# Kernel optimization log

Hardware: AMD Instinct MI355X
Metric: run time of the kernel (lower is better)

## Reference

```python
import jax, jax.numpy as jnp
import numpy as np

NUM_NODES = 100000
NUM_EDGES = 3200000
NHEADS = 8


def setup_inputs() -> dict:
    key = jax.random.key(0)
    k1, k2 = jax.random.split(key)
    edge_scores = jax.random.normal(k1, (NUM_EDGES, NHEADS, 1), dtype=jnp.float32)
    dst = jax.random.randint(k2, (NUM_EDGES,), 0, NUM_NODES, dtype=jnp.int32)
    gain = jnp.ones((NHEADS, 1), dtype=jnp.float32)
    bias = jnp.zeros((NHEADS, 1), dtype=jnp.float32)
    return {"edge_scores": edge_scores, "gain": gain, "bias": bias,
            "dst": dst, "num_nodes": NUM_NODES}


def reference(edge_scores, gain, bias, dst, num_nodes):
    # Per-destination-node mean/std normalization of incoming-edge scores
    # (EdgeNorm), then per-head gain/bias.
    # edge_scores: (E, H, 1); dst: (E,) int; gain/bias: (H, 1)
    ones = jnp.ones_like(edge_scores)
    counts = jax.ops.segment_sum(ones, dst, num_segments=num_nodes)        # (N,H,1)
    sums = jax.ops.segment_sum(edge_scores, dst, num_segments=num_nodes)   # (N,H,1)
    means = sums / jnp.maximum(counts, 1.0)
    residual = edge_scores - means[dst]                                    # (E,H,1)
    var_sum = jax.ops.segment_sum(residual * residual, dst, num_segments=num_nodes)
    stdev = jnp.sqrt(var_sum / counts)  # NaN only at zero-degree nodes (never gathered)
    inv_stdev = 1.0 / jnp.maximum(stdev, 1e-5)                             # (N,H,1)
    normalized = residual * inv_stdev[dst]                                 # (E,H,1)
    return gain * normalized + bias
```

## Files before the change

kernel.cpp:

```cpp
#include <hip/hip_runtime.h>


#define NHEADS  8
#define KSHIFT  9
#define KNODES  512
#define NNODES  100000
#define NB      196
#define CBLK    2048
#define CHMAX   1600
#define PARTS   8
#define SLMAX   2560
#define ACCW    17

__global__ __launch_bounds__(256)
void count_kernel(const int* __restrict__ dst, unsigned* __restrict__ counts,
                  int p0, int p1, int chunk) {
    __shared__ unsigned hist[NB];
    for (int i = threadIdx.x; i < NB; i += 256) hist[i] = 0u;
    __syncthreads();
    const int blk = blockIdx.x;
    const int s0 = p0 + blk * chunk;
    const int s1 = min(s0 + chunk, p1);
    for (int i = s0 + (int)threadIdx.x * 4; i < s1; i += 256 * 4) {
        if (i + 4 <= s1) {
            int4 d = *reinterpret_cast<const int4*>(dst + i);
            atomicAdd(&hist[(unsigned)d.x >> KSHIFT], 1u);
            atomicAdd(&hist[(unsigned)d.y >> KSHIFT], 1u);
            atomicAdd(&hist[(unsigned)d.z >> KSHIFT], 1u);
            atomicAdd(&hist[(unsigned)d.w >> KSHIFT], 1u);
        } else {
            for (int j = i; j < s1; ++j)
                atomicAdd(&hist[(unsigned)dst[j] >> KSHIFT], 1u);
        }
    }
    __syncthreads();
    for (int b = threadIdx.x; b < NB; b += 256)
        counts[(size_t)b * CBLK + blk] = hist[b];
}

__global__ __launch_bounds__(256)
void scan_kernel(unsigned* __restrict__ counts, unsigned* __restrict__ totals) {
    __shared__ unsigned sc[256];
    const int b = blockIdx.x;
    const size_t base = (size_t)b * CBLK + (size_t)threadIdx.x * 8;
    uint4 v0 = *reinterpret_cast<uint4*>(counts + base);
    uint4 v1 = *reinterpret_cast<uint4*>(counts + base + 4);
    unsigned s = v0.x + v0.y + v0.z + v0.w + v1.x + v1.y + v1.z + v1.w;
    sc[threadIdx.x] = s;
    __syncthreads();
    for (int off = 1; off < 256; off <<= 1) {
        unsigned t = (threadIdx.x >= (unsigned)off) ? sc[threadIdx.x - off] : 0u;
        __syncthreads();
        sc[threadIdx.x] += t;
        __syncthreads();
    }
    unsigned e = sc[threadIdx.x] - s;
    uint4 o0, o1;
    o0.x = e;            o0.y = o0.x + v0.x;
    o0.z = o0.y + v0.y;  o0.w = o0.z + v0.z;
    o1.x = o0.w + v0.w;  o1.y = o1.x + v1.x;
    o1.z = o1.y + v1.y;  o1.w = o1.z + v1.z;
    *reinterpret_cast<uint4*>(counts + base) = o0;
    *reinterpret_cast<uint4*>(counts + base + 4) = o1;
    if (threadIdx.x == 255) totals[b] = sc[255];
}

__global__ __launch_bounds__(256)
void base_kernel(const unsigned* __restrict__ totals, unsigned* __restrict__ base) {
    __shared__ unsigned sc[256];
    unsigned v = (threadIdx.x < NB) ? totals[threadIdx.x] : 0u;
    sc[threadIdx.x] = v;
    __syncthreads();
    for (int off = 1; off < 256; off <<= 1) {
        unsigned t = (threadIdx.x >= (unsigned)off) ? sc[threadIdx.x - off] : 0u;
        __syncthreads();
        sc[threadIdx.x] += t;
        __syncthreads();
    }
    if (threadIdx.x < NB) base[threadIdx.x] = sc[threadIdx.x] - v;
}

__global__ __launch_bounds__(256)
void scatter_kernel(const int* __restrict__ dst,
                    const unsigned* __restrict__ counts,
                    const unsigned* __restrict__ base,
                    const float* __restrict__ scores,
                    float* __restrict__ payload,
                    unsigned short* __restrict__ nidx,
                    int p0, int p1, int chunk, unsigned capE) {
    __shared__ unsigned hist[256];
    __shared__ unsigned pfx[NB];
    __shared__ unsigned lofs[NB];
    __shared__ unsigned gbase[NB];
    __shared__ unsigned ord[CHMAX];
    const int blk = blockIdx.x;
    const int s0 = p0 + blk * chunk;
    const int s1 = min(s0 + chunk, p1);
    const int n  = s1 - s0;

    hist[threadIdx.x] = 0u;
    __syncthreads();
    for (int i = s0 + (int)threadIdx.x * 4; i < s1; i += 256 * 4) {
        if (i + 4 <= s1) {
            int4 d = *reinterpret_cast<const int4*>(dst + i);
            atomicAdd(&hist[(unsigned)d.x >> KSHIFT], 1u);
            atomicAdd(&hist[(unsigned)d.y >> KSHIFT], 1u);
            atomicAdd(&hist[(unsigned)d.z >> KSHIFT], 1u);
            atomicAdd(&hist[(unsigned)d.w >> KSHIFT], 1u);
        } else {
            for (int j = i; j < s1; ++j)
                atomicAdd(&hist[(unsigned)dst[j] >> KSHIFT], 1u);
        }
    }
    __syncthreads();
    unsigned myc = hist[threadIdx.x];
    for (int off = 1; off < 256; off <<= 1) {
        unsigned t = (threadIdx.x >= (unsigned)off) ? hist[threadIdx.x - off] : 0u;
        __syncthreads();
        hist[threadIdx.x] += t;
        __syncthreads();
    }
    unsigned excl = hist[threadIdx.x] - myc;
    if (threadIdx.x < NB) {
        pfx[threadIdx.x]  = excl;
        lofs[threadIdx.x] = excl;
        gbase[threadIdx.x] =
            base[threadIdx.x] + counts[(size_t)threadIdx.x * CBLK + blk];
    }
    __syncthreads();
    for (int i = s0 + (int)threadIdx.x; i < s1; i += 256) {
        int d = dst[i];
        unsigned b = (unsigned)d >> KSHIFT;
        unsigned pos = atomicAdd(&lofs[b], 1u);
        if (pos < (unsigned)CHMAX)
            ord[pos] = (unsigned)(i - s0) |
                       ((unsigned)(d & (KNODES - 1)) << 12) | (b << 21);
    }
    __syncthreads();
    for (int p = (int)threadIdx.x; p < n; p += 256) {
        unsigned r = ord[p];
        int el       = (int)(r & 0xFFFu);
        unsigned nib = (r >> 12) & 0x1FFu;
        unsigned b   = r >> 21;
        unsigned gi  = gbase[b] + (unsigned)p - pfx[b];
        if (gi >= capE) continue;
        const float4* ps = reinterpret_cast<const float4*>(
            scores + (size_t)(s0 + el) * NHEADS);
        float4 x0 = ps[0], x1 = ps[1];
        float4* pd = reinterpret_cast<float4*>(payload + (size_t)gi * NHEADS);
        pd[0] = x0;
        pd[1] = x1;
        nidx[gi] = (unsigned short)nib;
    }
}

__global__ __launch_bounds__(512)
void stats_kernel(const float* __restrict__ payload,
                  const unsigned short* __restrict__ nidx,
                  const unsigned* __restrict__ totals,
                  const unsigned* __restrict__ baseb,
                  float* __restrict__ nodeacc) {
    __shared__ unsigned hist[KNODES];
    __shared__ unsigned seg[KNODES + 1];
    __shared__ unsigned cur[KNODES];
    __shared__ unsigned sc[512];
    __shared__ unsigned short sidx[SLMAX];

    const int part  = blockIdx.x;
    const int b     = blockIdx.y;
    const int total = (int)totals[b];
    const int rs    = (int)baseb[b];
    const int sliceLen = (total + PARTS - 1) / PARTS;
    const int l0 = min(total, part * sliceLen);
    const int l1 = min(total, l0 + sliceLen);
    const int n  = l1 - l0;
    if (n <= 0) return;
    const int gs0 = rs + l0;

    const int tid = (int)threadIdx.x;
    if (tid < KNODES) hist[tid] = 0u;
    __syncthreads();
    for (int i = tid; i < n; i += 512) {
        if (i >= SLMAX) break;
        unsigned k = (unsigned)nidx[gs0 + i] & (KNODES - 1);
        atomicAdd(&hist[k], 1u);
    }
    __syncthreads();
    unsigned v = hist[tid];
    sc[tid] = v;
    __syncthreads();
    for (int off = 1; off < 512; off <<= 1) {
        unsigned t = (tid >= off) ? sc[tid - off] : 0u;
        __syncthreads();
        sc[tid] += t;
        __syncthreads();
    }
    unsigned excl = sc[tid] - v;
    seg[tid] = excl;
    cur[tid] = excl;
    if (tid == 511) seg[KNODES] = sc[511];
    __syncthreads();
    for (int i = tid; i < n; i += 512) {
        if (i >= SLMAX) break;
        unsigned k = (unsigned)nidx[gs0 + i] & (KNODES - 1);
        unsigned pos = atomicAdd(&cur[k], 1u);
        if (pos < (unsigned)SLMAX) sidx[pos] = (unsigned short)i;
    }
    __syncthreads();

    const int wv   = tid >> 6;
    const int lane = tid & 63;
    const int grp  = lane >> 3;
    const int h    = lane & 7;
    for (int k = wv; k < KNODES; k += 8) {
        int ss = (int)seg[k];
        int ee = (int)seg[k + 1];
        int cc = ee - ss;
        if (cc <= 0) continue;
        float sv = 0.f, sw = 0.f;
        for (int j = grp; j < cc; j += 8) {
            int li = (int)sidx[ss + j];
            float x = payload[(size_t)(gs0 + li) * NHEADS + h];
            sv += x;
            sw = fmaf(x, x, sw);
        }
        sv += __shfl_xor(sv, 8);  sw += __shfl_xor(sw, 8);
        sv += __shfl_xor(sv, 16); sw += __shfl_xor(sw, 16);
        sv += __shfl_xor(sv, 32); sw += __shfl_xor(sw, 32);
        int gnode = b * KNODES + k;
        if (lane < ACCW && gnode < NNODES) {
            float val = (lane < 8) ? sv : ((lane < 16) ? sw : (float)cc);
            atomicAdd(&nodeacc[(size_t)gnode * ACCW + lane], val);
        }
    }
}

__global__ __launch_bounds__(256)
void coeff_kernel(const float* __restrict__ nodeacc,
                  const float* __restrict__ gain,
                  const float* __restrict__ bias,
                  float* __restrict__ AB, int total) {
    int i = blockIdx.x * 256 + threadIdx.x;
    if (i >= total) return;
    int node = i >> 3, h = i & 7;
    const float* acc = nodeacc + (size_t)node * ACCW;
    float s = acc[h];
    float q = acc[8 + h];
    float c = acc[16];
    float cm   = fmaxf(c, 1.0f);
    float mean = s / cm;
    float var  = fmaxf(q - s * mean, 0.0f);
    float inv  = 1.0f / fmaxf(sqrtf(var / cm), 1e-5f);
    float a = gain[h] * inv;
    AB[(size_t)node * 16 + h]     = a;
    AB[(size_t)node * 16 + 8 + h] = fmaf(-a, mean, bias[h]);
}

__global__ __launch_bounds__(256)
void edge_out_kernel(const float* __restrict__ scores,
                     const int* __restrict__ dst,
                     const float* __restrict__ AB,
                     float* __restrict__ out,
                     int num_edges) {
    int e = blockIdx.x * 256 + threadIdx.x;
    if (e >= num_edges) return;
    int d = dst[e];
    const float4* px  = reinterpret_cast<const float4*>(scores + (size_t)e * NHEADS);
    const float4* pab = reinterpret_cast<const float4*>(AB + (size_t)d * 16);
    float4 x0 = px[0], x1 = px[1];
    float4 a0 = pab[0], a1 = pab[1];
    float4 b0 = pab[2], b1 = pab[3];
    float4 o0, o1;
    o0.x = fmaf(a0.x, x0.x, b0.x);
    o0.y = fmaf(a0.y, x0.y, b0.y);
    o0.z = fmaf(a0.z, x0.z, b0.z);
    o0.w = fmaf(a0.w, x0.w, b0.w);
    o1.x = fmaf(a1.x, x1.x, b1.x);
    o1.y = fmaf(a1.y, x1.y, b1.y);
    o1.z = fmaf(a1.z, x1.z, b1.z);
    o1.w = fmaf(a1.w, x1.w, b1.w);
    float4* po = reinterpret_cast<float4*>(out + (size_t)e * NHEADS);
    po[0] = o0;
    po[1] = o1;
}

__global__ void edge_stats_fallback(const float* __restrict__ scores,
                                    const int* __restrict__ dst,
                                    float* __restrict__ sums,
                                    float* __restrict__ sumsq,
                                    int* __restrict__ counts,
                                    int num_edges) {
    int e = blockIdx.x * blockDim.x + threadIdx.x;
    if (e >= num_edges) return;
    int d = dst[e];
    const float4* p = reinterpret_cast<const float4*>(scores + (size_t)e * NHEADS);
    float4 x0 = p[0], x1 = p[1];
    float* s = sums  + (size_t)d * NHEADS;
    float* q = sumsq + (size_t)d * NHEADS;
    atomicAdd(s + 0, x0.x); atomicAdd(s + 1, x0.y);
    atomicAdd(s + 2, x0.z); atomicAdd(s + 3, x0.w);
    atomicAdd(s + 4, x1.x); atomicAdd(s + 5, x1.y);
    atomicAdd(s + 6, x1.z); atomicAdd(s + 7, x1.w);
    atomicAdd(q + 0, x0.x * x0.x); atomicAdd(q + 1, x0.y * x0.y);
    atomicAdd(q + 2, x0.z * x0.z); atomicAdd(q + 3, x0.w * x0.w);
    atomicAdd(q + 4, x1.x * x1.x); atomicAdd(q + 5, x1.y * x1.y);
    atomicAdd(q + 6, x1.z * x1.z); atomicAdd(q + 7, x1.w * x1.w);
    atomicAdd(counts + d, 1);
}

__global__ void coeff_fallback(const float* __restrict__ sums,
                               const float* __restrict__ sumsq,
                               const int* __restrict__ counts,
                               const float* __restrict__ gain,
                               const float* __restrict__ bias,
                               float* __restrict__ AB, int total) {
    int i = blockIdx.x * blockDim.x + threadIdx.x;
    if (i >= total) return;
    int h = i & (NHEADS - 1);
    int node = i >> 3;
    float cm = fmaxf((float)counts[node], 1.0f);
    float s = sums[i];
    float mean = s / cm;
    float var_sum = fmaxf(sumsq[i] - s * mean, 0.0f);
    float inv = 1.0f / fmaxf(sqrtf(var_sum / cm), 1e-5f);
    float a = gain[h] * inv;
    AB[(size_t)node * 16 + h]     = a;
    AB[(size_t)node * 16 + 8 + h] = fmaf(-a, mean, bias[h]);
}

extern "C" void kernel_launch(void* const* d_in, const int* in_sizes, int n_in,
                              void* d_out, int out_size, void* d_ws, size_t ws_size,
                              hipStream_t stream) {
    const float* scores = (const float*)d_in[0];
    const float* gain   = (const float*)d_in[1];
    const float* bias   = (const float*)d_in[2];
    const int*   dst    = (const int*)d_in[3];

    const int E  = in_sizes[3];
    const int N  = NNODES;
    const int NH = N * NHEADS;
    const int B  = 256;

    size_t off = 0;
    float* AB = (float*)d_ws;                          off += (size_t)N * 16 * 4;
    off = (off + 255) & ~(size_t)255;
    unsigned* counts = (unsigned*)((char*)d_ws + off); off += (size_t)NB * CBLK * 4;
    off = (off + 255) & ~(size_t)255;
    unsigned* totals = (unsigned*)((char*)d_ws + off); off += (size_t)NB * 4;
    off = (off + 255) & ~(size_t)255;
    unsigned* baseb  = (unsigned*)((char*)d_ws + off); off += (size_t)NB * 4;
    off = (off + 255) & ~(size_t)255;
    float* nodeacc   = (float*)((char*)d_ws + off);    off += (size_t)N * ACCW * 4;
    off = (off + 255) & ~(size_t)255;
    const size_t fixed = off;

    int P = 0, chunk = 0;
    size_t payOff = 0, nixOff = 0;
    size_t passCap = 0;
    const int cand[4] = {1, 2, 4, 8};
    for (int ci = 0; ci < 4; ++ci) {
        int p = cand[ci];
        long long perPass = ((long long)E + p - 1) / p;
        long long ch = (((perPass + CBLK - 1) / CBLK) + 3) & ~3LL;
        if (ch > CHMAX) continue;
        size_t passE = (size_t)ch * CBLK;
        size_t po = fixed;
        size_t no = (po + passE * NHEADS * 4 + 255) & ~(size_t)255;
        size_t need = no + passE * 2;
        if (need <= ws_size) {
            P = p; chunk = (int)ch; payOff = po; nixOff = no; passCap = passE;
            break;
        }
    }

    if (P) {
        float* payload = (float*)((char*)d_ws + payOff);
        unsigned short* nidx = (unsigned short*)((char*)d_ws + nixOff);
        hipMemsetAsync(nodeacc, 0, (size_t)N * ACCW * 4, stream);
        for (int pass = 0; pass < P; ++pass) {
            int p0 = pass * chunk * CBLK;
            if (p0 >= E) break;
            int p1 = min(E, p0 + chunk * CBLK);
            count_kernel<<<CBLK, B, 0, stream>>>(dst, counts, p0, p1, chunk);
            scan_kernel<<<NB, B, 0, stream>>>(counts, totals);
            base_kernel<<<1, B, 0, stream>>>(totals, baseb);
            scatter_kernel<<<CBLK, B, 0, stream>>>(dst, counts, baseb, scores,
                                                   payload, nidx, p0, p1, chunk,
                                                   (unsigned)passCap);
            dim3 gs(PARTS, NB);
            stats_kernel<<<gs, 512, 0, stream>>>(payload, nidx, totals, baseb,
                                                 nodeacc);
        }
        coeff_kernel<<<(NH + B - 1) / B, B, 0, stream>>>(nodeacc, gain, bias, AB, NH);
        edge_out_kernel<<<(E + B - 1) / B, B, 0, stream>>>(scores, dst, AB,
                                                           (float*)d_out, E);
    } else {
        float* sums  = (float*)((char*)d_ws + (size_t)N * 16 * 4);
        float* sumsq = sums + NH;
        int*   cnts  = (int*)(sumsq + NH);
        hipMemsetAsync(sums, 0,
                       (size_t)(2 * NH) * sizeof(float) + (size_t)N * sizeof(int), stream);
        int blocks_e = (E + B - 1) / B;
        edge_stats_fallback<<<blocks_e, B, 0, stream>>>(scores, dst, sums, sumsq, cnts, E);
        coeff_fallback<<<(NH + B - 1) / B, B, 0, stream>>>(sums, sumsq, cnts, gain, bias, AB, NH);
        edge_out_kernel<<<blocks_e, B, 0, stream>>>(scores, dst, AB, (float*)d_out, E);
    }
}
```

Baseline: 441.2 us.

## Stage bucket payload in LDS, halve slice sizes, split node count accumulator

The stats kernel now copies its contiguous payload slice into shared memory with coalesced float4 loads and then reads it through the sorted index from LDS, instead of doing scattered global gathers. Count-block and slice sizes are halved while PARTS doubles, so the per-block LDS slice fits, and the scan kernel is adjusted to 4 elements per thread. The 17-float accumulator record is split into a 16-float aligned sum/sumsq array plus a separate count array. This adds about 40KB of LDS per block, which can lower occupancy, and slices longer than SLMAX are now silently truncated.

```diff
diff --git a/kernel.cpp b/kernel.cpp
--- a/kernel.cpp
+++ b/kernel.cpp
@@ -6,11 +6,10 @@
 #define KNODES  512
 #define NNODES  100000
 #define NB      196
-#define CBLK    2048
-#define CHMAX   1600
-#define PARTS   8
-#define SLMAX   2560
-#define ACCW    17
+#define CBLK    1024
+#define CHMAX   3200
+#define PARTS   16
+#define SLMAX   1280
 
 __global__ __launch_bounds__(256)
 void count_kernel(const int* __restrict__ dst, unsigned* __restrict__ counts,
@@ -42,10 +41,9 @@
 void scan_kernel(unsigned* __restrict__ counts, unsigned* __restrict__ totals) {
     __shared__ unsigned sc[256];
     const int b = blockIdx.x;
-    const size_t base = (size_t)b * CBLK + (size_t)threadIdx.x * 8;
-    uint4 v0 = *reinterpret_cast<uint4*>(counts + base);
-    uint4 v1 = *reinterpret_cast<uint4*>(counts + base + 4);
-    unsigned s = v0.x + v0.y + v0.z + v0.w + v1.x + v1.y + v1.z + v1.w;
+    const size_t base = (size_t)b * CBLK + (size_t)threadIdx.x * 4;
+    uint4 v = *reinterpret_cast<uint4*>(counts + base);
+    unsigned s = v.x + v.y + v.z + v.w;
     sc[threadIdx.x] = s;
     __syncthreads();
     for (int off = 1; off < 256; off <<= 1) {
@@ -54,14 +52,13 @@
         sc[threadIdx.x] += t;
         __syncthreads();
     }
-    unsigned e = sc[threadIdx.x] - s;
-    uint4 o0, o1;
-    o0.x = e;            o0.y = o0.x + v0.x;
-    o0.z = o0.y + v0.y;  o0.w = o0.z + v0.z;
-    o1.x = o0.w + v0.w;  o1.y = o1.x + v1.x;
-    o1.z = o1.y + v1.y;  o1.w = o1.z + v1.z;
-    *reinterpret_cast<uint4*>(counts + base) = o0;
-    *reinterpret_cast<uint4*>(counts + base + 4) = o1;
+    unsigned excl = sc[threadIdx.x] - s;
+    uint4 o;
+    o.x = excl;
+    o.y = excl + v.x;
+    o.z = o.y + v.y;
+    o.w = o.z + v.z;
+    *reinterpret_cast<uint4*>(counts + base) = o;
     if (threadIdx.x == 255) totals[b] = sc[255];
 }
 
@@ -159,7 +156,9 @@
                   const unsigned short* __restrict__ nidx,
                   const unsigned* __restrict__ totals,
                   const unsigned* __restrict__ baseb,
-                  float* __restrict__ nodeacc) {
+                  float* __restrict__ nodeacc,
+                  float* __restrict__ nodecnt) {
+    __shared__ float pay[SLMAX * NHEADS];
     __shared__ unsigned hist[KNODES];
     __shared__ unsigned seg[KNODES + 1];
     __shared__ unsigned cur[KNODES];
@@ -173,15 +172,22 @@
     const int sliceLen = (total + PARTS - 1) / PARTS;
     const int l0 = min(total, part * sliceLen);
     const int l1 = min(total, l0 + sliceLen);
-    const int n  = l1 - l0;
+    int n = l1 - l0;
     if (n <= 0) return;
+    if (n > SLMAX) n = SLMAX;
     const int gs0 = rs + l0;
 
     const int tid = (int)threadIdx.x;
+    {
+        const float4* gp = reinterpret_cast<const float4*>(
+            payload + (size_t)gs0 * NHEADS);
+        float4* lp = reinterpret_cast<float4*>(pay);
+        const int nv = n * 2;
+        for (int i = tid; i < nv; i += 512) lp[i] = gp[i];
+    }
     if (tid < KNODES) hist[tid] = 0u;
     __syncthreads();
     for (int i = tid; i < n; i += 512) {
-        if (i >= SLMAX) break;
         unsigned k = (unsigned)nidx[gs0 + i] & (KNODES - 1);
         atomicAdd(&hist[k], 1u);
     }
@@ -201,7 +207,6 @@
     if (tid == 511) seg[KNODES] = sc[511];
     __syncthreads();
     for (int i = tid; i < n; i += 512) {
-        if (i >= SLMAX) break;
         unsigned k = (unsigned)nidx[gs0 + i] & (KNODES - 1);
         unsigned pos = atomicAdd(&cur[k], 1u);
         if (pos < (unsigned)SLMAX) sidx[pos] = (unsigned short)i;
@@ -220,7 +225,7 @@
         float sv = 0.f, sw = 0.f;
         for (int j = grp; j < cc; j += 8) {
             int li = (int)sidx[ss + j];
-            float x = payload[(size_t)(gs0 + li) * NHEADS + h];
+            float x = pay[li * NHEADS + h];
             sv += x;
             sw = fmaf(x, x, sw);
         }
@@ -228,25 +233,29 @@
         sv += __shfl_xor(sv, 16); sw += __shfl_xor(sw, 16);
         sv += __shfl_xor(sv, 32); sw += __shfl_xor(sw, 32);
         int gnode = b * KNODES + k;
-        if (lane < ACCW && gnode < NNODES) {
-            float val = (lane < 8) ? sv : ((lane < 16) ? sw : (float)cc);
-            atomicAdd(&nodeacc[(size_t)gnode * ACCW + lane], val);
+        if (gnode < NNODES) {
+            if (lane < 16)
+                atomicAdd(&nodeacc[(size_t)gnode * 16 + lane],
+                          (lane < 8) ? sv : sw);
+            else if (lane == 16)
+                atomicAdd(&nodecnt[gnode], (float)cc);
         }
     }
 }
 
 __global__ __launch_bounds__(256)
 void coeff_kernel(const float* __restrict__ nodeacc,
+                  const float* __restrict__ nodecnt,
                   const float* __restrict__ gain,
                   const float* __restrict__ bias,
                   float* __restrict__ AB, int total) {
     int i = blockIdx.x * 256 + threadIdx.x;
     if (i >= total) return;
     int node = i >> 3, h = i & 7;
-    const float* acc = nodeacc + (size_t)node * ACCW;
+    const float* acc = nodeacc + (size_t)node * 16;
     float s = acc[h];
     float q = acc[8 + h];
-    float c = acc[16];
+    float c = nodecnt[node];
     float cm   = fmaxf(c, 1.0f);
     float mean = s / cm;
     float var  = fmaxf(q - s * mean, 0.0f);
@@ -350,7 +359,9 @@
     off = (off + 255) & ~(size_t)255;
     unsigned* baseb  = (unsigned*)((char*)d_ws + off); off += (size_t)NB * 4;
     off = (off + 255) & ~(size_t)255;
-    float* nodeacc   = (float*)((char*)d_ws + off);    off += (size_t)N * ACCW * 4;
+    float* nodeacc   = (float*)((char*)d_ws + off);    off += (size_t)N * 16 * 4;
+    off = (off + 255) & ~(size_t)255;
+    float* nodecnt   = (float*)((char*)d_ws + off);    off += (size_t)N * 4;
     off = (off + 255) & ~(size_t)255;
     const size_t fixed = off;
 
@@ -376,7 +387,8 @@
     if (P) {
         float* payload = (float*)((char*)d_ws + payOff);
         unsigned short* nidx = (unsigned short*)((char*)d_ws + nixOff);
-        hipMemsetAsync(nodeacc, 0, (size_t)N * ACCW * 4, stream);
+        hipMemsetAsync(nodeacc, 0, (size_t)N * 16 * 4, stream);
+        hipMemsetAsync(nodecnt, 0, (size_t)N * 4, stream);
         for (int pass = 0; pass < P; ++pass) {
             int p0 = pass * chunk * CBLK;
             if (p0 >= E) break;
@@ -389,9 +401,10 @@
                                                    (unsigned)passCap);
             dim3 gs(PARTS, NB);
             stats_kernel<<<gs, 512, 0, stream>>>(payload, nidx, totals, baseb,
-                                                 nodeacc);
-        }
-        coeff_kernel<<<(NH + B - 1) / B, B, 0, stream>>>(nodeacc, gain, bias, AB, NH);
+                                                 nodeacc, nodecnt);
+        }
+        coeff_kernel<<<(NH + B - 1) / B, B, 0, stream>>>(nodeacc, nodecnt,
+                                                         gain, bias, AB, NH);
         edge_out_kernel<<<(E + B - 1) / B, B, 0, stream>>>(scores, dst, AB,
                                                            (float*)d_out, E);
     } else {
```

New measurement: 544.6 us. +23.4%, slower.
